# Kernel tuning notes

Measured on AMD Instinct MI355X. Metric: run time of the kernel, lower is better.

The kernel has to match this reference:

```python
import jax, jax.numpy as jnp
import numpy as np


def _bilinear_sample(v, gx, gy, H_, W_):
    # v: (B, H_, W_, nh, Cv); gx, gy: (B, Lq, nh, P) in [0,1] normalized coords.
    # Matches F.grid_sample(mode='bilinear', padding_mode='zeros', align_corners=False).
    x = gx * W_ - 0.5
    y = gy * H_ - 0.5
    x0 = jnp.floor(x)
    y0 = jnp.floor(y)
    dx = x - x0
    dy = y - y0
    x0i = x0.astype(jnp.int32)
    y0i = y0.astype(jnp.int32)
    nh = v.shape[3]
    hidx = jnp.arange(nh)[None, :, None]  # broadcast over (Lq, nh, P)

    def corner(yi, xi):
        valid = (yi >= 0) & (yi < H_) & (xi >= 0) & (xi < W_)
        yc = jnp.clip(yi, 0, H_ - 1)
        xc = jnp.clip(xi, 0, W_ - 1)
        gather = jax.vmap(lambda vb, yb, xb: vb[yb, xb, hidx])  # -> (B, Lq, nh, P, Cv)
        return gather(v, yc, xc) * valid[..., None].astype(v.dtype)

    v00 = corner(y0i, x0i)
    v01 = corner(y0i, x0i + 1)
    v10 = corner(y0i + 1, x0i)
    v11 = corner(y0i + 1, x0i + 1)
    wx0 = (1.0 - dx)[..., None]
    wx1 = dx[..., None]
    wy0 = (1.0 - dy)[..., None]
    wy1 = dy[..., None]
    return wy0 * (wx0 * v00 + wx1 * v01) + wy1 * (wx0 * v10 + wx1 * v11)


def setup_inputs() -> dict:
    key = jax.random.key(0)
    ks = jax.random.split(key, 10)
    C, NH, NL, NP = 256, 8, 4, 4
    B = 1
    shapes = np.array([[128, 128], [64, 64], [32, 32], [16, 16]], dtype=np.int64)
    L_in = int((shapes[:, 0] * shapes[:, 1]).sum())  # 21760
    Lq = L_in
    lsi = np.concatenate([[0], np.cumsum(shapes[:, 0] * shapes[:, 1])[:-1]]).astype(np.int64)

    # sampling_offsets bias init (grid of directions scaled by point index), per _reset_parameters
    thetas = np.arange(NH, dtype=np.float32) * (2.0 * np.pi / NH)
    grid = np.stack([np.cos(thetas), np.sin(thetas)], -1)
    grid = grid / np.abs(grid).max(-1, keepdims=True)
    grid = np.tile(grid[:, None, None, :], (1, NL, NP, 1))
    grid = grid * (np.arange(NP, dtype=np.float32) + 1.0)[None, None, :, None]
    b_off = jnp.asarray(grid.reshape(-1))

    xav = float(np.sqrt(2.0 / (C + C)))
    return {
        "query": jax.random.normal(ks[0], (B, Lq, C), jnp.float32),
        "reference_points": jax.random.uniform(ks[1], (B, Lq, NL, 2), jnp.float32),
        "input_flatten": jax.random.normal(ks[2], (B, L_in, C), jnp.float32),
        "input_spatial_shapes": jnp.asarray(shapes),
        "input_level_start_index": jnp.asarray(lsi),
        "input_padding_mask": jnp.zeros((B, L_in), jnp.bool_),
        "W_off": 0.01 * jax.random.normal(ks[3], (C, NH * NL * NP * 2), jnp.float32),
        "b_off": b_off,
        "W_attn": 0.01 * jax.random.normal(ks[4], (C, NH * NL * NP), jnp.float32),
        "b_attn": jnp.zeros((NH * NL * NP,), jnp.float32),
        "W_v": xav * jax.random.normal(ks[5], (C, C), jnp.float32),
        "b_v": jnp.zeros((C,), jnp.float32),
        "W_out": xav * jax.random.normal(ks[6], (C, C), jnp.float32),
        "b_out": jnp.zeros((C,), jnp.float32),
    }


def reference(query, reference_points, input_flatten, input_spatial_shapes,
              input_level_start_index, input_padding_mask,
              W_off, b_off, W_attn, b_attn, W_v, b_v, W_out, b_out):
    shapes = np.asarray(input_spatial_shapes)  # static spatial shapes (host constants)
    B, Lq, C = query.shape
    NL = shapes.shape[0]
    NH = 8
    Cv = C // NH
    NP = b_off.shape[0] // (NH * NL * 2)

    value = input_flatten @ W_v + b_v
    value = jnp.where(input_padding_mask[..., None], 0.0, value)
    value = value.reshape(B, -1, NH, Cv)

    off = (query @ W_off + b_off).reshape(B, Lq, NH, NL, NP, 2)
    attn = (query @ W_attn + b_attn).reshape(B, Lq, NH, NL * NP)
    attn = jax.nn.softmax(attn, axis=-1).reshape(B, Lq, NH, NL, NP)

    # normalizer is (W, H) per level
    norm = jnp.stack([jnp.asarray(shapes[:, 1]), jnp.asarray(shapes[:, 0])], -1).astype(query.dtype)
    loc = reference_points[:, :, None, :, None, :] + off / norm[None, None, None, :, None, :]

    out = jnp.zeros((B, Lq, NH, Cv), query.dtype)
    start = 0
    for lvl in range(NL):
        H_, W_ = int(shapes[lvl, 0]), int(shapes[lvl, 1])
        v_l = value[:, start:start + H_ * W_].reshape(B, H_, W_, NH, Cv)
        start += H_ * W_
        g = loc[:, :, :, lvl]  # (B, Lq, NH, NP, 2)
        sampled = _bilinear_sample(v_l, g[..., 0], g[..., 1], H_, W_)  # (B, Lq, NH, NP, Cv)
        out = out + jnp.einsum('blhpc,blhp->blhc', sampled, attn[:, :, :, lvl])

    out = out.reshape(B, Lq, C) @ W_out + b_out
    return out  # dropout is identity in eval mode
```

## Files before the change

### kernel.cpp

```cpp
#include <hip/hip_runtime.h>
#include <hip/hip_bf16.h>
#include <hip/hip_fp16.h>


typedef _Float16 f16;
typedef _Float16 f16x8 __attribute__((ext_vector_type(8)));
typedef float    f32x4 __attribute__((ext_vector_type(4)));

__device__ __forceinline__ void g2lds16(const void* gp, void* lp) {
    __builtin_amdgcn_global_load_lds(
        (const __attribute__((address_space(1))) unsigned int*)gp,
        (__attribute__((address_space(3))) unsigned int*)lp, 16, 0, 0);
}

template <bool HALF_OUT, bool MASKED>
__global__ __launch_bounds__(512) void gemm_f32a(
    const float* __restrict__ Af,
    const f16* __restrict__ Bt,
    const float* __restrict__ bias,
    void* __restrict__ Cout, int M, int N,
    const unsigned char* __restrict__ mask)
{
    __shared__ __align__(16) f16 As[2][64 * 64];
    __shared__ __align__(16) f16 Bs[2][128 * 64];

    const int tid  = threadIdx.x;
    const int m0   = blockIdx.y * 64, n0 = blockIdx.x * 128;
    const int lane = tid & 63, wid = tid >> 6;
    const int wm   = (wid >> 2) * 32, wn = (wid & 3) * 32;

    const int arow = tid >> 3;
    const int acb  = tid & 7;
    float4 ar[4][2];
#pragma unroll
    for (int g = 0; g < 4; ++g)
#pragma unroll
        for (int h2 = 0; h2 < 2; ++h2)
            ar[g][h2] = *reinterpret_cast<const float4*>(
                Af + (size_t)(m0 + arow) * 256 + g * 64 + acb * 8 + h2 * 4);

    f32x4 acc[2][2] = {};

    auto stageA = [&](int buf, int kt) {
        const int  g  = kt < 4 ? kt : (kt < 8 ? kt - 4 : kt - 8);
        const bool lo = (kt >= 4 && kt < 8);
        f16x8 v;
#pragma unroll
        for (int h2 = 0; h2 < 2; ++h2) {
            const float4 f = ar[g][h2];
            const float fv[4] = {f.x, f.y, f.z, f.w};
#pragma unroll
            for (int j = 0; j < 4; ++j) {
                const f16 hi = (f16)fv[j];
                v[h2 * 4 + j] = lo ? (f16)(fv[j] - (float)hi) : hi;
            }
        }
        const int cc = acb ^ (arow & 7);
        *reinterpret_cast<f16x8*>(&As[buf][arow * 64 + cc * 8]) = v;
    };
    const int sr  = tid >> 3;
    const int sch = tid & 7;
    auto stageB = [&](int buf, int kt) {
#pragma unroll
        for (int p = 0; p < 2; ++p) {
            const int r  = p * 64 + sr;
            const int gc = (sch ^ (r & 7)) << 3;
            g2lds16(Bt + (size_t)(n0 + r) * 768 + kt * 64 + gc,
                    &Bs[buf][r * 64 + sch * 8]);
        }
    };

    stageB(0, 0);
    stageA(0, 0);

#pragma unroll
    for (int kt = 0; kt < 12; ++kt) {
        const int cur = kt & 1;
        __syncthreads();

        f16x8 av[2][2], bv[2][2];
#pragma unroll
        for (int kf = 0; kf < 2; ++kf) {
            const int kch = kf * 4 + (lane >> 4);
#pragma unroll
            for (int mf = 0; mf < 2; ++mf) {
                const int row = wm + mf * 16 + (lane & 15);
                av[kf][mf] = *(const f16x8*)&As[cur][row * 64 + ((kch ^ (row & 7)) << 3)];
            }
#pragma unroll
            for (int nf = 0; nf < 2; ++nf) {
                const int row = wn + nf * 16 + (lane & 15);
                bv[kf][nf] = *(const f16x8*)&Bs[cur][row * 64 + ((kch ^ (row & 7)) << 3)];
            }
        }
        if (kt < 11) { stageB(cur ^ 1, kt + 1); stageA(cur ^ 1, kt + 1); }
#pragma unroll
        for (int kf = 0; kf < 2; ++kf)
#pragma unroll
            for (int mf = 0; mf < 2; ++mf)
#pragma unroll
                for (int nf = 0; nf < 2; ++nf)
                    acc[mf][nf] = __builtin_amdgcn_mfma_f32_16x16x32_f16(
                        av[kf][mf], bv[kf][nf], acc[mf][nf], 0, 0, 0);
    }

#pragma unroll
    for (int mf = 0; mf < 2; ++mf) {
        const int rb = m0 + wm + mf * 16 + ((lane >> 4) << 2);
#pragma unroll
        for (int nf = 0; nf < 2; ++nf) {
            const int col = n0 + wn + nf * 16 + (lane & 15);
            const float bc = bias[col];
#pragma unroll
            for (int j = 0; j < 4; ++j) {
                const int row = rb + j;
                float v = acc[mf][nf][j] + bc;
                if (MASKED) v = mask[row] ? 0.f : v;
                if (HALF_OUT)
                    ((__half*)Cout)[(size_t)row * N + col] = __float2half(v);
                else
                    ((float*)Cout)[(size_t)row * N + col] = v;
            }
        }
    }
}

__global__ __launch_bounds__(256) void prep_kernel(
    const float* __restrict__ Wv,   const float* __restrict__ Woff,
    const float* __restrict__ Wattn,const float* __restrict__ Wout,
    const float* __restrict__ boff, const float* __restrict__ battn,
    f16* __restrict__ Btv, f16* __restrict__ Btoa, f16* __restrict__ Btout,
    float* __restrict__ boa)
{
    const int i = blockIdx.x * 256 + threadIdx.x;
    constexpr int S0 = 256 * 768, S1 = 256 * 768, S2 = 128 * 768, S3 = 256 * 768;
    if (i < S0) {
        const int n = i / 768, k = i - n * 768, ks = k & 255;
        const float w = Wv[(size_t)ks * 256 + n];
        const f16 h = (f16)w;
        Btv[i] = (k < 512) ? h : (f16)(w - (float)h);
    } else if (i < S0 + S1) {
        const int j = i - S0;
        const int n = j / 768, k = j - n * 768, ks = k & 255;
        const float w = Woff[(size_t)ks * 256 + n];
        const f16 h = (f16)w;
        Btoa[j] = (k < 512) ? h : (f16)(w - (float)h);
    } else if (i < S0 + S1 + S2) {
        const int j = i - S0 - S1;
        const int n = j / 768, k = j - n * 768, ks = k & 255;
        const float w = Wattn[(size_t)ks * 128 + n];
        const f16 h = (f16)w;
        Btoa[(size_t)(256 + n) * 768 + k] = (k < 512) ? h : (f16)(w - (float)h);
    } else if (i < S0 + S1 + S2 + S3) {
        const int j = i - S0 - S1 - S2;
        const int n = j / 768, k = j - n * 768, ks = k & 255;
        const float w = Wout[(size_t)ks * 256 + n];
        const f16 h = (f16)w;
        Btout[j] = (k < 512) ? h : (f16)(w - (float)h);
    } else if (i < S0 + S1 + S2 + S3 + 384) {
        const int j = i - S0 - S1 - S2 - S3;
        boa[j] = (j < 256) ? boff[j] : battn[j - 256];
    }
}

__global__ __launch_bounds__(256) void msda_sample_v3(
    const __half* __restrict__ value,
    const float* __restrict__ offattn,
    const float* __restrict__ refp,
    float* __restrict__ pre)
{
    __shared__ float s_off[2][256];
    __shared__ float s_ref[2][8];
    __shared__ __align__(16) float s_w[2][576];
    __shared__ __align__(16) int   s_i[2][576];

    const int q0 = blockIdx.x * 2, tid = threadIdx.x;
#pragma unroll
    for (int j = 0; j < 2; ++j) {
        const int idx = tid + j * 256;
        const int ql = idx >> 8, col = idx & 255;
        s_off[ql][col] = offattn[(size_t)(q0 + ql) * 384 + col];
    }
    if (tid < 16) s_ref[tid >> 3][tid & 7] = refp[(size_t)(q0 + (tid >> 3)) * 8 + (tid & 7)];
    __syncthreads();

    {
        const int ql = tid >> 7, slot = tid & 127;
        const int h = slot >> 4, pp = slot & 15, l = pp >> 2, p = pp & 3;
        float v = offattn[(size_t)(q0 + ql) * 384 + 256 + slot];
        float mx = v;
#pragma unroll
        for (int o = 1; o < 16; o <<= 1) mx = fmaxf(mx, __shfl_xor(mx, o, 16));
        const float e = expf(v - mx);
        float s = e;
#pragma unroll
        for (int o = 1; o < 16; o <<= 1) s += __shfl_xor(s, o, 16);
        const float a = e / s;

        const int HW_[4]  = {128, 64, 32, 16};
        const int LSI_[4] = {0, 16384, 20480, 21504};
        const int   Wi = HW_[l];
        const float Wf = (float)Wi;
        const float rx = s_ref[ql][l * 2 + 0], ry = s_ref[ql][l * 2 + 1];
        const float ox = s_off[ql][h * 32 + l * 8 + p * 2 + 0];
        const float oy = s_off[ql][h * 32 + l * 8 + p * 2 + 1];
        const float x = (rx + ox / Wf) * Wf - 0.5f;
        const float y = (ry + oy / Wf) * Wf - 0.5f;
        const float x0f = floorf(x), y0f = floorf(y);
        const float dx = x - x0f, dy = y - y0f;
        const int x0 = (int)x0f, y0 = (int)y0f;
        const int x1 = x0 + 1, y1 = y0 + 1;
        const float vx0 = (x0 >= 0 && x0 < Wi) ? 1.f : 0.f;
        const float vx1 = (x1 >= 0 && x1 < Wi) ? 1.f : 0.f;
        const float vy0 = (y0 >= 0 && y0 < Wi) ? 1.f : 0.f;
        const float vy1 = (y1 >= 0 && y1 < Wi) ? 1.f : 0.f;
        const int xc0 = min(max(x0, 0), Wi - 1), xc1 = min(max(x1, 0), Wi - 1);
        const int yc0 = min(max(y0, 0), Wi - 1), yc1 = min(max(y1, 0), Wi - 1);
        const int base = LSI_[l];
        const int eI = h * 72 + pp * 4;
        s_i[ql][eI + 0] = (base + yc0 * Wi + xc0) * 512;
        s_i[ql][eI + 1] = (base + yc0 * Wi + xc1) * 512;
        s_i[ql][eI + 2] = (base + yc1 * Wi + xc0) * 512;
        s_i[ql][eI + 3] = (base + yc1 * Wi + xc1) * 512;
        s_w[ql][eI + 0] = a * (1.f - dy) * (1.f - dx) * vy0 * vx0;
        s_w[ql][eI + 1] = a * (1.f - dy) * dx         * vy0 * vx1;
        s_w[ql][eI + 2] = a * dy         * (1.f - dx) * vy1 * vx0;
        s_w[ql][eI + 3] = a * dy         * dx         * vy1 * vx1;
    }
    __syncthreads();

    const int ql = tid >> 7, slot = tid & 127;
    const int h = slot >> 4, cp = slot & 15;
    const int lb = h * 64 + cp * 4;
    const char* __restrict__ vbase = (const char*)value;
    float acc0 = 0.f, acc1 = 0.f;
#pragma unroll
    for (int pp = 0; pp < 16; ++pp) {
        const int eI = h * 72 + pp * 4;
        const int4   idx = *reinterpret_cast<const int4*>(&s_i[ql][eI]);
        const float4 w   = *reinterpret_cast<const float4*>(&s_w[ql][eI]);
        const __half2 v0 = *reinterpret_cast<const __half2*>(vbase + (idx.x + lb));
        const __half2 v1 = *reinterpret_cast<const __half2*>(vbase + (idx.y + lb));
        const __half2 v2 = *reinterpret_cast<const __half2*>(vbase + (idx.z + lb));
        const __half2 v3 = *reinterpret_cast<const __half2*>(vbase + (idx.w + lb));
        acc0 = fmaf(w.x, __half2float(v0.x), acc0);
        acc1 = fmaf(w.x, __half2float(v0.y), acc1);
        acc0 = fmaf(w.y, __half2float(v1.x), acc0);
        acc1 = fmaf(w.y, __half2float(v1.y), acc1);
        acc0 = fmaf(w.z, __half2float(v2.x), acc0);
        acc1 = fmaf(w.z, __half2float(v2.y), acc1);
        acc0 = fmaf(w.w, __half2float(v3.x), acc0);
        acc1 = fmaf(w.w, __half2float(v3.y), acc1);
    }
    float2 o; o.x = acc0; o.y = acc1;
    *reinterpret_cast<float2*>(&pre[(size_t)(q0 + ql) * 256 + h * 32 + cp * 2]) = o;
}

extern "C" void kernel_launch(void* const* d_in, const int* in_sizes, int n_in,
                              void* d_out, int out_size, void* d_ws, size_t ws_size,
                              hipStream_t stream)
{
    const float*         query  = (const float*)d_in[0];
    const float*         refp   = (const float*)d_in[1];
    const float*         inF    = (const float*)d_in[2];
    const unsigned char* mask   = (const unsigned char*)d_in[5];
    const float*         W_off  = (const float*)d_in[6];
    const float*         b_off  = (const float*)d_in[7];
    const float*         W_attn = (const float*)d_in[8];
    const float*         b_attn = (const float*)d_in[9];
    const float*         W_v    = (const float*)d_in[10];
    const float*         b_v    = (const float*)d_in[11];
    const float*         W_out  = (const float*)d_in[12];
    const float*         b_out  = (const float*)d_in[13];
    float*               out    = (float*)d_out;

    const int M = in_sizes[0] / 256;
    if (M % 128 != 0) return;

    const size_t SZ_VAL = (size_t)M * 256 * sizeof(__half);
    const size_t SZ_OA  = (size_t)M * 384 * sizeof(float);
    const size_t SZ_PRE = (size_t)M * 256 * sizeof(float);
    const size_t SZ_BTV = 256 * 768 * sizeof(f16);
    const size_t SZ_BTO = 384 * 768 * sizeof(f16);
    char* w = (char*)d_ws;
    __half* valueH = (__half*)w;                   w += SZ_VAL;
    float*  offattn= (float*)w;                    w += SZ_OA;
    float*  pre    = (float*)w;                    w += SZ_PRE;
    f16*    Btv    = (f16*)w;                      w += SZ_BTV;
    f16*    Btoa   = (f16*)w;                      w += SZ_BTO;
    f16*    Btout  = (f16*)w;                      w += SZ_BTV;
    float*  boa    = (float*)w;                    w += 512 * sizeof(float);
    if ((size_t)(w - (char*)d_ws) > ws_size) return;

    const dim3 blk256(256), blk512(512);
    const int prep_total = 3 * 256 * 768 + 128 * 768 + 384;

    prep_kernel<<<dim3((prep_total + 255) / 256), blk256, 0, stream>>>(
        W_v, W_off, W_attn, W_out, b_off, b_attn, Btv, Btoa, Btout, boa);

    gemm_f32a<true, true><<<dim3(2, M / 64), blk512, 0, stream>>>(
        inF, Btv, b_v, valueH, M, 256, mask);

    gemm_f32a<false, false><<<dim3(3, M / 64), blk512, 0, stream>>>(
        query, Btoa, boa, offattn, M, 384, nullptr);

    msda_sample_v3<<<dim3(M / 2), blk256, 0, stream>>>(valueH, offattn, refp, pre);

    gemm_f32a<false, false><<<dim3(2, M / 64), blk512, 0, stream>>>(
        pre, Btout, b_out, out, M, 256, nullptr);
}
```

Before: 225.6 us.

## Pre-split activations to f16 hi/lo, batch GEMMs, widen sampler loads

Adds a kernel that converts the input and query activations to f16 hi/lo split buffers up front, so the GEMMs stage A tiles with direct global-to-LDS loads instead of converting in registers. The value, offset and attention GEMMs are merged into one launch with 128x128 tiles and a single-buffered k loop of 24 steps. The sampler handles four queries per block, loads four halves per thread, and writes the hi/lo f16 operand for the output GEMM directly. It reuses the output buffer to hold offsets and A1 to hold the sampler result. This cuts launches and fp32 traffic but drops double buffering and adds an extra pass over the activations.

Result: slower. 239.5 us (+6.1%).

```diff
diff --git a/kernel.cpp b/kernel.cpp
--- a/kernel.cpp
+++ b/kernel.cpp
@@ -5,7 +5,9 @@
 
 typedef _Float16 f16;
 typedef _Float16 f16x8 __attribute__((ext_vector_type(8)));
+typedef _Float16 f16x4 __attribute__((ext_vector_type(4)));
 typedef float    f32x4 __attribute__((ext_vector_type(4)));
+typedef int      i32x2 __attribute__((ext_vector_type(2)));
 
 __device__ __forceinline__ void g2lds16(const void* gp, void* lp) {
     __builtin_amdgcn_global_load_lds(
@@ -14,123 +16,138 @@
 }
 
 template <bool HALF_OUT, bool MASKED>
-__global__ __launch_bounds__(512) void gemm_f32a(
-    const float* __restrict__ Af,
-    const f16* __restrict__ Bt,
+__device__ __forceinline__ void gemm_core(
+    const f16* __restrict__ A, const f16* __restrict__ Btb,
     const float* __restrict__ bias,
-    void* __restrict__ Cout, int M, int N,
-    const unsigned char* __restrict__ mask)
-{
-    __shared__ __align__(16) f16 As[2][64 * 64];
-    __shared__ __align__(16) f16 Bs[2][128 * 64];
-
-    const int tid  = threadIdx.x;
-    const int m0   = blockIdx.y * 64, n0 = blockIdx.x * 128;
-    const int lane = tid & 63, wid = tid >> 6;
-    const int wm   = (wid >> 2) * 32, wn = (wid & 3) * 32;
-
-    const int arow = tid >> 3;
-    const int acb  = tid & 7;
-    float4 ar[4][2];
-#pragma unroll
-    for (int g = 0; g < 4; ++g)
-#pragma unroll
-        for (int h2 = 0; h2 < 2; ++h2)
-            ar[g][h2] = *reinterpret_cast<const float4*>(
-                Af + (size_t)(m0 + arow) * 256 + g * 64 + acb * 8 + h2 * 4);
-
-    f32x4 acc[2][2] = {};
-
-    auto stageA = [&](int buf, int kt) {
-        const int  g  = kt < 4 ? kt : (kt < 8 ? kt - 4 : kt - 8);
-        const bool lo = (kt >= 4 && kt < 8);
-        f16x8 v;
-#pragma unroll
-        for (int h2 = 0; h2 < 2; ++h2) {
-            const float4 f = ar[g][h2];
-            const float fv[4] = {f.x, f.y, f.z, f.w};
-#pragma unroll
-            for (int j = 0; j < 4; ++j) {
-                const f16 hi = (f16)fv[j];
-                v[h2 * 4 + j] = lo ? (f16)(fv[j] - (float)hi) : hi;
-            }
-        }
-        const int cc = acb ^ (arow & 7);
-        *reinterpret_cast<f16x8*>(&As[buf][arow * 64 + cc * 8]) = v;
-    };
-    const int sr  = tid >> 3;
-    const int sch = tid & 7;
-    auto stageB = [&](int buf, int kt) {
+    void* __restrict__ C, int ldc, int coff,
+    const unsigned char* __restrict__ mask, int m0,
+    f16* __restrict__ As, f16* __restrict__ Bs)
+{
+    const int tid = threadIdx.x, lane = tid & 63, wid = tid >> 6;
+    const int wm = (wid >> 1) * 64, wn = (wid & 1) * 64;
+    f32x4 acc[4][4] = {};
+
+    const int sr_ = tid >> 2;
+    const int sch = tid & 3;
+
+    for (int kt = 0; kt < 24; ++kt) {
+        const int kA = (kt < 16 ? kt : kt - 16) * 32;
+        const int kB = kt * 32;
 #pragma unroll
         for (int p = 0; p < 2; ++p) {
-            const int r  = p * 64 + sr;
-            const int gc = (sch ^ (r & 7)) << 3;
-            g2lds16(Bt + (size_t)(n0 + r) * 768 + kt * 64 + gc,
-                    &Bs[buf][r * 64 + sch * 8]);
-        }
-    };
-
-    stageB(0, 0);
-    stageA(0, 0);
-
-#pragma unroll
-    for (int kt = 0; kt < 12; ++kt) {
-        const int cur = kt & 1;
+            const int r  = p * 64 + sr_;
+            const int gc = (sch ^ ((r >> 1) & 3)) << 3;
+            g2lds16(A + (size_t)(m0 + r) * 512 + kA + gc, &As[r * 32 + sch * 8]);
+        }
+#pragma unroll
+        for (int p = 0; p < 2; ++p) {
+            const int r  = p * 64 + sr_;
+            const int gc = (sch ^ ((r >> 1) & 3)) << 3;
+            g2lds16(Btb + (size_t)r * 768 + kB + gc, &Bs[r * 32 + sch * 8]);
+        }
         __syncthreads();
 
-        f16x8 av[2][2], bv[2][2];
-#pragma unroll
-        for (int kf = 0; kf < 2; ++kf) {
-            const int kch = kf * 4 + (lane >> 4);
-#pragma unroll
-            for (int mf = 0; mf < 2; ++mf) {
-                const int row = wm + mf * 16 + (lane & 15);
-                av[kf][mf] = *(const f16x8*)&As[cur][row * 64 + ((kch ^ (row & 7)) << 3)];
-            }
-#pragma unroll
-            for (int nf = 0; nf < 2; ++nf) {
-                const int row = wn + nf * 16 + (lane & 15);
-                bv[kf][nf] = *(const f16x8*)&Bs[cur][row * 64 + ((kch ^ (row & 7)) << 3)];
-            }
-        }
-        if (kt < 11) { stageB(cur ^ 1, kt + 1); stageA(cur ^ 1, kt + 1); }
-#pragma unroll
-        for (int kf = 0; kf < 2; ++kf)
-#pragma unroll
-            for (int mf = 0; mf < 2; ++mf)
-#pragma unroll
-                for (int nf = 0; nf < 2; ++nf)
-                    acc[mf][nf] = __builtin_amdgcn_mfma_f32_16x16x32_f16(
-                        av[kf][mf], bv[kf][nf], acc[mf][nf], 0, 0, 0);
-    }
-
-#pragma unroll
-    for (int mf = 0; mf < 2; ++mf) {
+        f16x8 av[4], bv[4];
+        const int kch = lane >> 4;
+#pragma unroll
+        for (int mf = 0; mf < 4; ++mf) {
+            const int row = wm + mf * 16 + (lane & 15);
+            av[mf] = *(const f16x8*)&As[row * 32 + ((kch ^ ((row >> 1) & 3)) << 3)];
+        }
+#pragma unroll
+        for (int nf = 0; nf < 4; ++nf) {
+            const int row = wn + nf * 16 + (lane & 15);
+            bv[nf] = *(const f16x8*)&Bs[row * 32 + ((kch ^ ((row >> 1) & 3)) << 3)];
+        }
+#pragma unroll
+        for (int mf = 0; mf < 4; ++mf)
+#pragma unroll
+            for (int nf = 0; nf < 4; ++nf)
+                acc[mf][nf] = __builtin_amdgcn_mfma_f32_16x16x32_f16(
+                    av[mf], bv[nf], acc[mf][nf], 0, 0, 0);
+        __syncthreads();
+    }
+
+#pragma unroll
+    for (int mf = 0; mf < 4; ++mf) {
         const int rb = m0 + wm + mf * 16 + ((lane >> 4) << 2);
 #pragma unroll
-        for (int nf = 0; nf < 2; ++nf) {
-            const int col = n0 + wn + nf * 16 + (lane & 15);
-            const float bc = bias[col];
+        for (int nf = 0; nf < 4; ++nf) {
+            const int nl = wn + nf * 16 + (lane & 15);
+            const float bc = bias[nl];
 #pragma unroll
             for (int j = 0; j < 4; ++j) {
                 const int row = rb + j;
                 float v = acc[mf][nf][j] + bc;
                 if (MASKED) v = mask[row] ? 0.f : v;
                 if (HALF_OUT)
-                    ((__half*)Cout)[(size_t)row * N + col] = __float2half(v);
+                    ((__half*)C)[(size_t)row * ldc + coff + nl] = __float2half(v);
                 else
-                    ((float*)Cout)[(size_t)row * N + col] = v;
+                    ((float*)C)[(size_t)row * ldc + coff + nl] = v;
             }
         }
     }
+}
+
+__global__ __launch_bounds__(256) void gemm_batch1(
+    const f16* __restrict__ A1, const f16* __restrict__ A2,
+    const f16* __restrict__ Btv, const f16* __restrict__ Btoa,
+    const float* __restrict__ b_v, const float* __restrict__ b_off,
+    const float* __restrict__ b_attn,
+    __half* __restrict__ valueH, float* __restrict__ outF,
+    float* __restrict__ logitF, const unsigned char* __restrict__ mask)
+{
+    __shared__ __align__(16) f16 As[128 * 32];
+    __shared__ __align__(16) f16 Bs[128 * 32];
+    const int bx = blockIdx.x, m0 = blockIdx.y * 128;
+    if (bx < 2)
+        gemm_core<true, true>(A1, Btv + (size_t)bx * 128 * 768, b_v + bx * 128,
+                              valueH, 256, bx * 128, mask, m0, As, Bs);
+    else if (bx < 4)
+        gemm_core<false, false>(A2, Btoa + (size_t)(bx - 2) * 128 * 768,
+                                b_off + (bx - 2) * 128, outF, 256,
+                                (bx - 2) * 128, nullptr, m0, As, Bs);
+    else
+        gemm_core<false, false>(A2, Btoa + (size_t)256 * 768, b_attn,
+                                logitF, 128, 0, nullptr, m0, As, Bs);
+}
+
+__global__ __launch_bounds__(256) void gemm_batch2(
+    const f16* __restrict__ preA, const f16* __restrict__ Btout,
+    const float* __restrict__ b_out, float* __restrict__ outF)
+{
+    __shared__ __align__(16) f16 As[128 * 32];
+    __shared__ __align__(16) f16 Bs[128 * 32];
+    const int bx = blockIdx.x, m0 = blockIdx.y * 128;
+    gemm_core<false, false>(preA, Btout + (size_t)bx * 128 * 768,
+                            b_out + bx * 128, outF, 256, bx * 128,
+                            nullptr, m0, As, Bs);
+}
+
+__global__ __launch_bounds__(256) void convA2_kernel(
+    const float* __restrict__ inF, const float* __restrict__ query,
+    f16* __restrict__ A1, f16* __restrict__ A2, int perT)
+{
+    const int i = blockIdx.x * 256 + threadIdx.x;
+    const float* __restrict__ src = (i < perT) ? inF : query;
+    f16* __restrict__ dst = (i < perT) ? A1 : A2;
+    const int ii = (i < perT) ? i : i - perT;
+    if (ii >= perT) return;
+    const int m = ii >> 6, k4 = (ii & 63) << 2;
+    const float4 v = reinterpret_cast<const float4*>(src)[ii];
+    f16x4 hi, lo;
+    hi.x = (f16)v.x; lo.x = (f16)(v.x - (float)hi.x);
+    hi.y = (f16)v.y; lo.y = (f16)(v.y - (float)hi.y);
+    hi.z = (f16)v.z; lo.z = (f16)(v.z - (float)hi.z);
+    hi.w = (f16)v.w; lo.w = (f16)(v.w - (float)hi.w);
+    *reinterpret_cast<f16x4*>(&dst[(size_t)m * 512 + k4])       = hi;
+    *reinterpret_cast<f16x4*>(&dst[(size_t)m * 512 + 256 + k4]) = lo;
 }
 
 __global__ __launch_bounds__(256) void prep_kernel(
     const float* __restrict__ Wv,   const float* __restrict__ Woff,
     const float* __restrict__ Wattn,const float* __restrict__ Wout,
-    const float* __restrict__ boff, const float* __restrict__ battn,
-    f16* __restrict__ Btv, f16* __restrict__ Btoa, f16* __restrict__ Btout,
-    float* __restrict__ boa)
+    f16* __restrict__ Btv, f16* __restrict__ Btoa, f16* __restrict__ Btout)
 {
     const int i = blockIdx.x * 256 + threadIdx.x;
     constexpr int S0 = 256 * 768, S1 = 256 * 768, S2 = 128 * 768, S3 = 256 * 768;
@@ -157,37 +174,37 @@
         const float w = Wout[(size_t)ks * 256 + n];
         const f16 h = (f16)w;
         Btout[j] = (k < 512) ? h : (f16)(w - (float)h);
-    } else if (i < S0 + S1 + S2 + S3 + 384) {
-        const int j = i - S0 - S1 - S2 - S3;
-        boa[j] = (j < 256) ? boff[j] : battn[j - 256];
-    }
-}
-
-__global__ __launch_bounds__(256) void msda_sample_v3(
+    }
+}
+
+__global__ __launch_bounds__(256) void msda_sample_v4(
     const __half* __restrict__ value,
-    const float* __restrict__ offattn,
+    const float* __restrict__ offF,
+    const float* __restrict__ logitF,
     const float* __restrict__ refp,
-    float* __restrict__ pre)
-{
-    __shared__ float s_off[2][256];
-    __shared__ float s_ref[2][8];
-    __shared__ __align__(16) float s_w[2][576];
-    __shared__ __align__(16) int   s_i[2][576];
-
-    const int q0 = blockIdx.x * 2, tid = threadIdx.x;
+    f16* __restrict__ preA)
+{
+    __shared__ float s_off[4][256];
+    __shared__ float s_ref[4][8];
+    __shared__ __align__(16) float s_w[4][576];
+    __shared__ __align__(16) int   s_i[4][576];
+
+    const int q0 = blockIdx.x * 4, tid = threadIdx.x;
+#pragma unroll
+    for (int j = 0; j < 4; ++j) {
+        const int idx = tid + j * 256;
+        const int ql = idx >> 8, col = idx & 255;
+        s_off[ql][col] = offF[(size_t)(q0 + ql) * 256 + col];
+    }
+    if (tid < 32) s_ref[tid >> 3][tid & 7] = refp[(size_t)(q0 + (tid >> 3)) * 8 + (tid & 7)];
+    __syncthreads();
+
 #pragma unroll
     for (int j = 0; j < 2; ++j) {
         const int idx = tid + j * 256;
-        const int ql = idx >> 8, col = idx & 255;
-        s_off[ql][col] = offattn[(size_t)(q0 + ql) * 384 + col];
-    }
-    if (tid < 16) s_ref[tid >> 3][tid & 7] = refp[(size_t)(q0 + (tid >> 3)) * 8 + (tid & 7)];
-    __syncthreads();
-
-    {
-        const int ql = tid >> 7, slot = tid & 127;
+        const int ql = idx >> 7, slot = idx & 127;
         const int h = slot >> 4, pp = slot & 15, l = pp >> 2, p = pp & 3;
-        float v = offattn[(size_t)(q0 + ql) * 384 + 256 + slot];
+        float v = logitF[(size_t)(q0 + ql) * 128 + slot];
         float mx = v;
 #pragma unroll
         for (int o = 1; o < 16; o <<= 1) mx = fmaxf(mx, __shfl_xor(mx, o, 16));
@@ -229,31 +246,34 @@
     }
     __syncthreads();
 
-    const int ql = tid >> 7, slot = tid & 127;
-    const int h = slot >> 4, cp = slot & 15;
-    const int lb = h * 64 + cp * 4;
+    const int ql = tid >> 6, slot = tid & 63;
+    const int h = slot >> 3, c8 = (slot & 7) << 2;
+    const int lb = (h * 32 + c8) * 2;
     const char* __restrict__ vbase = (const char*)value;
-    float acc0 = 0.f, acc1 = 0.f;
+    f32x4 acc = {0.f, 0.f, 0.f, 0.f};
 #pragma unroll
     for (int pp = 0; pp < 16; ++pp) {
         const int eI = h * 72 + pp * 4;
         const int4   idx = *reinterpret_cast<const int4*>(&s_i[ql][eI]);
-        const float4 w   = *reinterpret_cast<const float4*>(&s_w[ql][eI]);
-        const __half2 v0 = *reinterpret_cast<const __half2*>(vbase + (idx.x + lb));
-        const __half2 v1 = *reinterpret_cast<const __half2*>(vbase + (idx.y + lb));
-        const __half2 v2 = *reinterpret_cast<const __half2*>(vbase + (idx.z + lb));
-        const __half2 v3 = *reinterpret_cast<const __half2*>(vbase + (idx.w + lb));
-        acc0 = fmaf(w.x, __half2float(v0.x), acc0);
-        acc1 = fmaf(w.x, __half2float(v0.y), acc1);
-        acc0 = fmaf(w.y, __half2float(v1.x), acc0);
-        acc1 = fmaf(w.y, __half2float(v1.y), acc1);
-        acc0 = fmaf(w.z, __half2float(v2.x), acc0);
-        acc1 = fmaf(w.z, __half2float(v2.y), acc1);
-        acc0 = fmaf(w.w, __half2float(v3.x), acc0);
-        acc1 = fmaf(w.w, __half2float(v3.y), acc1);
-    }
-    float2 o; o.x = acc0; o.y = acc1;
-    *reinterpret_cast<float2*>(&pre[(size_t)(q0 + ql) * 256 + h * 32 + cp * 2]) = o;
+        const float4 wv  = *reinterpret_cast<const float4*>(&s_w[ql][eI]);
+        const i32x2 r0 = *reinterpret_cast<const i32x2*>(vbase + (idx.x + lb));
+        const i32x2 r1 = *reinterpret_cast<const i32x2*>(vbase + (idx.y + lb));
+        const i32x2 r2 = *reinterpret_cast<const i32x2*>(vbase + (idx.z + lb));
+        const i32x2 r3 = *reinterpret_cast<const i32x2*>(vbase + (idx.w + lb));
+        acc += wv.x * __builtin_convertvector(__builtin_bit_cast(f16x4, r0), f32x4);
+        acc += wv.y * __builtin_convertvector(__builtin_bit_cast(f16x4, r1), f32x4);
+        acc += wv.z * __builtin_convertvector(__builtin_bit_cast(f16x4, r2), f32x4);
+        acc += wv.w * __builtin_convertvector(__builtin_bit_cast(f16x4, r3), f32x4);
+    }
+    const int q = q0 + ql;
+    f16x4 hi, lo;
+#pragma unroll
+    for (int j = 0; j < 4; ++j) {
+        hi[j] = (f16)acc[j];
+        lo[j] = (f16)(acc[j] - (float)hi[j]);
+    }
+    *reinterpret_cast<f16x4*>(&preA[(size_t)q * 512 + h * 32 + c8])       = hi;
+    *reinterpret_cast<f16x4*>(&preA[(size_t)q * 512 + 256 + h * 32 + c8]) = lo;
 }
 
 extern "C" void kernel_launch(void* const* d_in, const int* in_sizes, int n_in,
@@ -272,40 +292,39 @@
     const float*         b_v    = (const float*)d_in[11];
     const float*         W_out  = (const float*)d_in[12];
     const float*         b_out  = (const float*)d_in[13];
-    float*               out    = (float*)d_out;
+    float*               outF   = (float*)d_out;
 
     const int M = in_sizes[0] / 256;
     if (M % 128 != 0) return;
 
+    const size_t SZ_A   = (size_t)M * 512 * sizeof(f16);
     const size_t SZ_VAL = (size_t)M * 256 * sizeof(__half);
-    const size_t SZ_OA  = (size_t)M * 384 * sizeof(float);
-    const size_t SZ_PRE = (size_t)M * 256 * sizeof(float);
-    const size_t SZ_BTV = 256 * 768 * sizeof(f16);
-    const size_t SZ_BTO = 384 * 768 * sizeof(f16);
+    const size_t SZ_LG  = (size_t)M * 128 * sizeof(float);
     char* w = (char*)d_ws;
+    f16*    A1     = (f16*)w;                      w += SZ_A;
+    f16*    A2     = (f16*)w;                      w += SZ_A;
     __half* valueH = (__half*)w;                   w += SZ_VAL;
-    float*  offattn= (float*)w;                    w += SZ_OA;
-    float*  pre    = (float*)w;                    w += SZ_PRE;
-    f16*    Btv    = (f16*)w;                      w += SZ_BTV;
-    f16*    Btoa   = (f16*)w;                      w += SZ_BTO;
-    f16*    Btout  = (f16*)w;                      w += SZ_BTV;
-    float*  boa    = (float*)w;                    w += 512 * sizeof(float);
+    float*  logitF = (float*)w;                    w += SZ_LG;
+    f16*    Btv    = (f16*)w;                      w += 256 * 768 * sizeof(f16);
+    f16*    Btoa   = (f16*)w;                      w += 384 * 768 * sizeof(f16);
+    f16*    Btout  = (f16*)w;                      w += 256 * 768 * sizeof(f16);
     if ((size_t)(w - (char*)d_ws) > ws_size) return;
 
-    const dim3 blk256(256), blk512(512);
-    const int prep_total = 3 * 256 * 768 + 128 * 768 + 384;
+    const dim3 blk256(256);
+    const int prep_total = (256 + 384 + 256) * 768;
+    const int perT = M * 64;
 
     prep_kernel<<<dim3((prep_total + 255) / 256), blk256, 0, stream>>>(
-        W_v, W_off, W_attn, W_out, b_off, b_attn, Btv, Btoa, Btout, boa);
-
-    gemm_f32a<true, true><<<dim3(2, M / 64), blk512, 0, stream>>>(
-        inF, Btv, b_v, valueH, M, 256, mask);
-
-    gemm_f32a<false, false><<<dim3(3, M / 64), blk512, 0, stream>>>(
-        query, Btoa, boa, offattn, M, 384, nullptr);
-
-    msda_sample_v3<<<dim3(M / 2), blk256, 0, stream>>>(valueH, offattn, refp, pre);
-
-    gemm_f32a<false, false><<<dim3(2, M / 64), blk512, 0, stream>>>(
-        pre, Btout, b_out, out, M, 256, nullptr);
-}
+        W_v, W_off, W_attn, W_out, Btv, Btoa, Btout);
+
+    convA2_kernel<<<dim3((2 * perT + 255) / 256), blk256, 0, stream>>>(
+        inF, query, A1, A2, perT);
+
+    gemm_batch1<<<dim3(5, M / 128), blk256, 0, stream>>>(
+        A1, A2, Btv, Btoa, b_v, b_off, b_attn, valueH, outF, logitF, mask);
+
+    msda_sample_v4<<<dim3(M / 4), blk256, 0, stream>>>(
+        valueH, outF, logitF, refp, A1);
+
+    gemm_batch2<<<dim3(2, M / 128), blk256, 0, stream>>>(A1, Btout, b_out, outF);
+}
```
